# Optimization experiments

Measured on AMD Instinct MI355X. Metric: run time of the kernel, lower is better.

## Reference

```python
import jax, jax.numpy as jnp
import numpy as np

NH = 8       # num_heads
EDIM = 256   # embedding_dim (also per-head dim in this module)
BS, SQL = 4, 1024


def setup_inputs() -> dict:
    key = jax.random.key(0)
    ks = jax.random.split(key, 5)
    scale_in = 1.0 / np.sqrt(EDIM)
    scale_out = 1.0 / np.sqrt(NH * EDIM)
    return {
        "x": jax.random.normal(ks[0], (BS, SQL, EDIM), dtype=jnp.float32),
        "w_attn": jax.random.normal(ks[1], (NH * 3 * EDIM, EDIM), dtype=jnp.float32) * scale_in,
        "b_attn": jax.random.normal(ks[2], (NH * 3 * EDIM,), dtype=jnp.float32) * scale_in,
        "w_out": jax.random.normal(ks[3], (EDIM, NH * EDIM), dtype=jnp.float32) * scale_out,
        "b_out": jax.random.normal(ks[4], (EDIM,), dtype=jnp.float32) * scale_out,
    }


def reference(x, w_attn, b_attn, w_out, b_out):
    bs, sql, edim = x.shape
    nh = NH
    # projections: (bs, sql, nh*3*edim); split into Q, K, V chunks of nh*edim
    proj = x @ w_attn.T + b_attn
    q, k, v = jnp.split(proj, 3, axis=-1)
    # Faithful to torch: raw view (bs, sql, nh*edim) -> (bs, nh, sql, edim),
    # a reinterpretation of memory, NOT a transpose.
    q = q.reshape(bs, nh, sql, edim)
    k = k.reshape(bs, nh, sql, edim)
    v = v.reshape(bs, nh, sql, edim)
    # scaled dot-product scores: (bs, nh, sql, sql)
    scores = jnp.einsum("bhqd,bhkd->bhqk", q, k) / jnp.sqrt(jnp.float32(edim))
    # causal mask: -inf strictly above the diagonal (equivalent to adding triu(-inf, 1))
    causal = jnp.tril(jnp.ones((sql, sql), dtype=bool))
    scores = jnp.where(causal, scores, -jnp.inf)
    attn = jax.nn.softmax(scores, axis=-1)
    out = jnp.einsum("bhqk,bhkd->bhqd", attn, v)
    # Faithful raw view back: (bs, nh, sql, edim) -> (bs, sql, nh*edim)
    out = out.reshape(bs, sql, nh * edim)
    return out @ w_out.T + b_out
```

## Files before the change

### kernel.cpp

```cpp
#include <hip/hip_runtime.h>

#define SQL  1024
#define EDIM 256
#define NHD  8
#define NKV  (NHD * 3 * EDIM)
#define MROWS (4 * SQL)

typedef short bf16x8 __attribute__((ext_vector_type(8)));
typedef float f32x4 __attribute__((ext_vector_type(4)));

__device__ __forceinline__ unsigned short f2bf(float f) {
  unsigned u = __float_as_uint(f);
  u += 0x7fff + ((u >> 16) & 1);
  return (unsigned short)(u >> 16);
}

__device__ __forceinline__ void g2lds16(const void* g, void* l) {
  __builtin_amdgcn_global_load_lds(
      (const __attribute__((address_space(1))) unsigned int*)g,
      (__attribute__((address_space(3))) unsigned int*)l, 16, 0, 0);
}

__device__ __forceinline__ void storev(float* p, float v) { *p = v; }
__device__ __forceinline__ void storev(unsigned short* p, float v) { *p = f2bf(v); }

__global__ __launch_bounds__(256) void cast3_bf16(
    const float* __restrict__ s0, unsigned short* __restrict__ d0, int n0,
    const float* __restrict__ s1, unsigned short* __restrict__ d1, int n1,
    const float* __restrict__ s2, unsigned short* __restrict__ d2, int n2) {
  int i = blockIdx.x * 256 + threadIdx.x;
  const float* s; unsigned short* d;
  if (i < n0) { s = s0; d = d0; }
  else if (i < n0 + n1) { i -= n0; s = s1; d = d1; }
  else { i -= n0 + n1; if (i >= n2) return; s = s2; d = d2; }
  float4 a = ((const float4*)s)[2 * i];
  float4 b = ((const float4*)s)[2 * i + 1];
  union { unsigned short u[8]; ulonglong2 v; } t;
  t.u[0] = f2bf(a.x); t.u[1] = f2bf(a.y); t.u[2] = f2bf(a.z); t.u[3] = f2bf(a.w);
  t.u[4] = f2bf(b.x); t.u[5] = f2bf(b.y); t.u[6] = f2bf(b.z); t.u[7] = f2bf(b.w);
  ((ulonglong2*)d)[i] = t.v;
}

template <int BM, int BN, typename OutT>
__global__ __launch_bounds__(256) void gemm_mfma(
    const unsigned short* __restrict__ A, const unsigned short* __restrict__ B,
    const float* __restrict__ bias, OutT* __restrict__ C,
    int M, int N, int K) {
  constexpr int TM = BM / 32, TN = BN / 32;
  __shared__ __align__(16) unsigned short As[2][BM * 32];
  __shared__ __align__(16) unsigned short Bs[2][BN * 32];
  const int tid = threadIdx.x;
  const int wave = tid >> 6, lane = tid & 63;
  const int quad = lane >> 4, l16 = lane & 15;
  const int wm = (wave >> 1) * (BM / 2), wn = (wave & 1) * (BN / 2);
  const int m0 = blockIdx.x * BM, n0 = blockIdx.y * BN;
  const int sw = (l16 >> 1) & 3;

  f32x4 acc[TM][TN];
  #pragma unroll
  for (int i = 0; i < TM; i++)
    #pragma unroll
    for (int j = 0; j < TN; j++) acc[i][j] = {0.f, 0.f, 0.f, 0.f};

  auto stage = [&](int k0, int bb) {
    #pragma unroll
    for (int it = 0; it < BM / 64; it++) {
      int flat = it * 256 + tid;
      int row = flat >> 2;
      int cg = (flat & 3) ^ ((row >> 1) & 3);
      g2lds16(A + (size_t)(m0 + row) * K + k0 + cg * 8, &As[bb][flat * 8]);
    }
    #pragma unroll
    for (int it = 0; it < BN / 64; it++) {
      int flat = it * 256 + tid;
      int row = flat >> 2;
      int cg = (flat & 3) ^ ((row >> 1) & 3);
      g2lds16(B + (size_t)(n0 + row) * K + k0 + cg * 8, &Bs[bb][flat * 8]);
    }
  };

  stage(0, 0);
  __syncthreads();
  for (int k0 = 0; k0 < K; k0 += 32) {
    const int bb = (k0 >> 5) & 1;
    if (k0 + 32 < K) stage(k0 + 32, bb ^ 1);
    bf16x8 af[TM], bf[TN];
    #pragma unroll
    for (int i = 0; i < TM; i++)
      af[i] = *(const bf16x8*)&As[bb][(wm + i * 16 + l16) * 32 + (quad ^ sw) * 8];
    #pragma unroll
    for (int j = 0; j < TN; j++)
      bf[j] = *(const bf16x8*)&Bs[bb][(wn + j * 16 + l16) * 32 + (quad ^ sw) * 8];
    #pragma unroll
    for (int i = 0; i < TM; i++)
      #pragma unroll
      for (int j = 0; j < TN; j++)
        acc[i][j] = __builtin_amdgcn_mfma_f32_16x16x32_bf16(af[i], bf[j], acc[i][j], 0, 0, 0);
    __syncthreads();
  }

  #pragma unroll
  for (int i = 0; i < TM; i++) {
    #pragma unroll
    for (int r = 0; r < 4; r++) {
      int m = m0 + wm + i * 16 + quad * 4 + r;
      #pragma unroll
      for (int j = 0; j < TN; j++) {
        int n = n0 + wn + j * 16 + l16;
        storev(&C[(size_t)m * N + n], acc[i][j][r] + bias[n]);
      }
    }
  }
}

__global__ __launch_bounds__(256) void transpose_v(
    const unsigned short* __restrict__ proj, unsigned short* __restrict__ vt) {
  __shared__ unsigned short T[64][66];
  const int tid = threadIdx.x;
  const int s0 = blockIdx.x * 64, d0 = blockIdx.y * 64, bh = blockIdx.z;
  const int b = bh >> 3, h = bh & 7;
  #pragma unroll
  for (int it = 0; it < 2; it++) {
    int c = it * 256 + tid;
    int sr = c >> 3, k8 = (c & 7) * 8;
    int s = s0 + sr;
    const unsigned short* src = proj + (size_t)(b * SQL + h * 128 + (s >> 3)) * NKV
                                + 2 * 2048 + (s & 7) * 256 + d0 + k8;
    *(ulonglong2*)&T[sr][k8] = *(const ulonglong2*)src;
  }
  __syncthreads();
  #pragma unroll
  for (int it = 0; it < 2; it++) {
    int c = it * 256 + tid;
    int dr = c >> 3, s8 = (c & 7) * 8;
    unsigned short tmp[8];
    #pragma unroll
    for (int j = 0; j < 8; j++) tmp[j] = T[s8 + j][dr];
    unsigned short* dst = vt + ((size_t)bh * EDIM + d0 + dr) * SQL + s0 + s8;
    *(ulonglong2*)dst = *(ulonglong2*)tmp;
  }
}

__global__ __launch_bounds__(512, 4) void attn_mfma(
    const unsigned short* __restrict__ proj,
    const unsigned short* __restrict__ vt,
    unsigned short* __restrict__ oflat) {
  __shared__ __align__(16) unsigned short lds[37888];
  unsigned short* Ps = lds + 32768;

  const int tid = threadIdx.x;
  const int wave = tid >> 6, lane = tid & 63;
  const int quad = lane >> 4, l16 = lane & 15;
  const int qs = wave >> 1;
  const int dh = wave & 1;
  const int slot = blockIdx.x & 255, round = blockIdx.x >> 8;
  const int bh = slot & 31;
  const int jj = slot >> 5;
  const int qt = round ? jj : 15 - jj;
  const int b = bh >> 3, h = bh & 7;
  const int q0 = qt * 64;

  #pragma unroll
  for (int it = 0; it < 4; it++) {
    int c = it * 512 + tid;
    int r = c >> 5, ch = (c & 31) ^ (r & 7);
    int s = q0 + r;
    g2lds16(proj + (size_t)(b * SQL + h * 128 + (s >> 3)) * NKV + (s & 7) * 256 + ch * 8,
            lds + c * 8);
  }
  __syncthreads();
  bf16x8 aq[8];
  const int qrow = qs * 16 + l16;
  #pragma unroll
  for (int kk = 0; kk < 8; kk++)
    aq[kk] = *(const bf16x8*)&lds[qrow * 256 + ((kk * 4 + quad) ^ (qrow & 7)) * 8];
  __syncthreads();

  f32x4 o[8];
  #pragma unroll
  for (int t = 0; t < 8; t++) o[t] = {0.f, 0.f, 0.f, 0.f};
  float l_r[4] = {0.f, 0.f, 0.f, 0.f};

  auto stage = [&](int kt, int bb) {
    unsigned short* KsB = lds + bb * 16384;
    unsigned short* VtB = KsB + 8192;
    #pragma unroll
    for (int it = 0; it < 2; it++) {
      int c = it * 512 + tid;
      int r = c >> 5, ch = (c & 31) ^ (r & 7);
      int s = kt * 32 + r;
      g2lds16(proj + (size_t)(b * SQL + h * 128 + (s >> 3)) * NKV + 2048 + (s & 7) * 256 + ch * 8,
              KsB + c * 8);
    }
    #pragma unroll
    for (int it = 0; it < 2; it++) {
      int c = it * 512 + tid;
      int d = c >> 2, ch = (c & 3) ^ (d & 3);
      g2lds16(vt + ((size_t)bh * EDIM + d) * SQL + kt * 32 + ch * 8, VtB + c * 8);
    }
  };

  const int nkt = 2 * qt + 2;
  stage(0, 0);
  __syncthreads();

  for (int kt = 0; kt < nkt; kt++) {
    const int bb = kt & 1;
    if (kt + 1 < nkt) stage(kt + 1, bb ^ 1);
    const unsigned short* KsB = lds + bb * 16384;
    const unsigned short* VtB = KsB + 8192;
    const bool live = (kt * 32 <= q0 + qs * 16 + 15);

    if (live) {
      f32x4 s0 = {0.f, 0.f, 0.f, 0.f}, s1 = {0.f, 0.f, 0.f, 0.f};
      #pragma unroll
      for (int kk = 0; kk < 8; kk++) {
        int ch = (kk * 4 + quad) ^ (l16 & 7);
        bf16x8 b0 = *(const bf16x8*)&KsB[l16 * 256 + ch * 8];
        bf16x8 b1 = *(const bf16x8*)&KsB[(16 + l16) * 256 + ch * 8];
        s0 = __builtin_amdgcn_mfma_f32_16x16x32_bf16(aq[kk], b0, s0, 0, 0, 0);
        s1 = __builtin_amdgcn_mfma_f32_16x16x32_bf16(aq[kk], b1, s1, 0, 0, 0);
      }

      const int kg0 = kt * 32 + l16, kg1 = kg0 + 16;
      unsigned short* PsW = Ps + wave * 640;
      #pragma unroll
      for (int r = 0; r < 4; r++) {
        int qg = q0 + qs * 16 + quad * 4 + r;
        float p0 = (kg0 <= qg) ? exp2f(s0[r] * 0.09016844f) : 0.f;
        float p1 = (kg1 <= qg) ? exp2f(s1[r] * 0.09016844f) : 0.f;
        l_r[r] += p0 + p1;
        PsW[(quad * 4 + r) * 40 + l16]      = f2bf(p0);
        PsW[(quad * 4 + r) * 40 + 16 + l16] = f2bf(p1);
      }

      bf16x8 ap = *(const bf16x8*)&PsW[l16 * 40 + quad * 8];
      #pragma unroll
      for (int tl = 0; tl < 8; tl++) {
        const int vrow = dh * 128 + tl * 16 + l16;
        bf16x8 bv = *(const bf16x8*)&VtB[vrow * 32 + (quad ^ (l16 & 3)) * 8];
        o[tl] = __builtin_amdgcn_mfma_f32_16x16x32_bf16(ap, bv, o[tl], 0, 0, 0);
      }
    }
    __syncthreads();
  }

  #pragma unroll
  for (int r = 0; r < 4; r++) {
    float l = l_r[r];
    #pragma unroll
    for (int off = 1; off < 16; off <<= 1) l += __shfl_xor(l, off);
    float inv = 1.0f / l;
    int s = q0 + qs * 16 + quad * 4 + r;
    unsigned short* dst = oflat + (size_t)(b * SQL + h * 128 + (s >> 3)) * 2048
                          + (s & 7) * 256 + dh * 128;
    #pragma unroll
    for (int tl = 0; tl < 8; tl++)
      dst[tl * 16 + l16] = f2bf(o[tl][r] * inv);
  }
}

extern "C" void kernel_launch(void* const* d_in, const int* in_sizes, int n_in,
                              void* d_out, int out_size, void* d_ws, size_t ws_size,
                              hipStream_t stream) {
  const float* x      = (const float*)d_in[0];
  const float* w_attn = (const float*)d_in[1];
  const float* b_attn = (const float*)d_in[2];
  const float* w_out  = (const float*)d_in[3];
  const float* b_out  = (const float*)d_in[4];
  float* out = (float*)d_out;

  char* p = (char*)d_ws;
  unsigned short* proj = (unsigned short*)p;  p += (size_t)MROWS * NKV * 2;
  unsigned short* obf  = (unsigned short*)p;  p += (size_t)MROWS * 2048 * 2;
  unsigned short* vtb  = (unsigned short*)p;  p += (size_t)32 * EDIM * SQL * 2;
  unsigned short* xb   = (unsigned short*)p;  p += (size_t)MROWS * EDIM * 2;
  unsigned short* wb   = (unsigned short*)p;  p += (size_t)NKV * EDIM * 2;
  unsigned short* wob  = (unsigned short*)p;

  const int n0 = MROWS * EDIM / 8;
  const int n1 = NKV * EDIM / 8;
  const int n2 = EDIM * 2048 / 8;
  cast3_bf16<<<(n0 + n1 + n2) / 256, 256, 0, stream>>>(x, xb, n0, w_attn, wb, n1,
                                                       w_out, wob, n2);

  gemm_mfma<128, 128, unsigned short><<<dim3(MROWS / 128, NKV / 128), 256, 0, stream>>>(
      xb, wb, b_attn, proj, MROWS, NKV, EDIM);
  transpose_v<<<dim3(SQL / 64, EDIM / 64, 32), 256, 0, stream>>>(proj, vtb);
  attn_mfma<<<512, 512, 0, stream>>>(proj, vtb, obf);
  gemm_mfma<64, 64, float><<<dim3(MROWS / 64, EDIM / 64), 256, 0, stream>>>(
      obf, wob, b_out, out, MROWS, EDIM, NHD * EDIM);
}
```

Before: 172.0 us.

## Split attention waves over key tiles instead of head-dim halves, merge partial outputs

The attention kernel now gives each wave pair a different 32-key tile from a 64-key staged pair, and each wave covers the full 256-wide head dim, instead of splitting the head dim across the pair. Before, both waves recomputed the same QK scores and softmax; now each wave computes scores only for its own keys. Partial outputs and row sums are merged through LDS at the end. V is pre-transposed into a tiled, swizzled layout so a whole key pair stages with contiguous loads. The cost is doubled accumulator registers and larger LDS, lowering occupancy from 4 to 2 blocks per CU, plus an extra reduction pass.

```diff
diff --git a/kernel.cpp b/kernel.cpp
--- a/kernel.cpp
+++ b/kernel.cpp
@@ -136,23 +136,28 @@
     unsigned short tmp[8];
     #pragma unroll
     for (int j = 0; j < 8; j++) tmp[j] = T[s8 + j][dr];
-    unsigned short* dst = vt + ((size_t)bh * EDIM + d0 + dr) * SQL + s0 + s8;
+    const int d = d0 + dr;
+    const int t = (s0 + s8) >> 5;
+    const int j = (s8 >> 3) & 3;
+    const int cj = j ^ ((d >> 1) & 3);
+    unsigned short* dst = vt + (((size_t)bh * 32 + t) * 1024 + d * 4 + cj) * 8;
     *(ulonglong2*)dst = *(ulonglong2*)tmp;
   }
 }
 
-__global__ __launch_bounds__(512, 4) void attn_mfma(
+__global__ __launch_bounds__(512, 2) void attn_mfma(
     const unsigned short* __restrict__ proj,
     const unsigned short* __restrict__ vt,
     unsigned short* __restrict__ oflat) {
-  __shared__ __align__(16) unsigned short lds[37888];
-  unsigned short* Ps = lds + 32768;
+  __shared__ __align__(16) unsigned short lds[70656];
+  __shared__ float lsumX[4][16];
+  unsigned short* Ps = lds + 65536;
 
   const int tid = threadIdx.x;
   const int wave = tid >> 6, lane = tid & 63;
   const int quad = lane >> 4, l16 = lane & 15;
   const int qs = wave >> 1;
-  const int dh = wave & 1;
+  const int p  = wave & 1;
   const int slot = blockIdx.x & 255, round = blockIdx.x >> 8;
   const int bh = slot & 31;
   const int jj = slot >> 5;
@@ -160,56 +165,55 @@
   const int b = bh >> 3, h = bh & 7;
   const int q0 = qt * 64;
 
+  auto stagepair = [&](int pr, int bb) {
+    unsigned short* B = lds + bb * 32768;
+    #pragma unroll
+    for (int it = 0; it < 4; it++) {
+      int c = it * 512 + tid;
+      int r = c >> 5, ch = (c & 31) ^ (r & 7);
+      int s = pr * 64 + r;
+      g2lds16(proj + (size_t)(b * SQL + h * 128 + (s >> 3)) * NKV + 2048 + (s & 7) * 256 + ch * 8,
+              B + c * 8);
+    }
+    const unsigned short* vsrc = vt + ((size_t)bh * 32 + pr * 2) * 8192;
+    #pragma unroll
+    for (int it = 0; it < 4; it++) {
+      int c = it * 512 + tid;
+      g2lds16(vsrc + c * 8, B + 16384 + c * 8);
+    }
+  };
+
+  stagepair(0, 0);
   #pragma unroll
   for (int it = 0; it < 4; it++) {
     int c = it * 512 + tid;
     int r = c >> 5, ch = (c & 31) ^ (r & 7);
     int s = q0 + r;
     g2lds16(proj + (size_t)(b * SQL + h * 128 + (s >> 3)) * NKV + (s & 7) * 256 + ch * 8,
-            lds + c * 8);
+            lds + 32768 + c * 8);
   }
   __syncthreads();
   bf16x8 aq[8];
   const int qrow = qs * 16 + l16;
   #pragma unroll
   for (int kk = 0; kk < 8; kk++)
-    aq[kk] = *(const bf16x8*)&lds[qrow * 256 + ((kk * 4 + quad) ^ (qrow & 7)) * 8];
-  __syncthreads();
-
-  f32x4 o[8];
-  #pragma unroll
-  for (int t = 0; t < 8; t++) o[t] = {0.f, 0.f, 0.f, 0.f};
+    aq[kk] = *(const bf16x8*)&lds[32768 + qrow * 256 + ((kk * 4 + quad) ^ (qrow & 7)) * 8];
+  __syncthreads();
+
+  f32x4 o[16];
+  #pragma unroll
+  for (int t = 0; t < 16; t++) o[t] = {0.f, 0.f, 0.f, 0.f};
   float l_r[4] = {0.f, 0.f, 0.f, 0.f};
 
-  auto stage = [&](int kt, int bb) {
-    unsigned short* KsB = lds + bb * 16384;
-    unsigned short* VtB = KsB + 8192;
-    #pragma unroll
-    for (int it = 0; it < 2; it++) {
-      int c = it * 512 + tid;
-      int r = c >> 5, ch = (c & 31) ^ (r & 7);
-      int s = kt * 32 + r;
-      g2lds16(proj + (size_t)(b * SQL + h * 128 + (s >> 3)) * NKV + 2048 + (s & 7) * 256 + ch * 8,
-              KsB + c * 8);
-    }
-    #pragma unroll
-    for (int it = 0; it < 2; it++) {
-      int c = it * 512 + tid;
-      int d = c >> 2, ch = (c & 3) ^ (d & 3);
-      g2lds16(vt + ((size_t)bh * EDIM + d) * SQL + kt * 32 + ch * 8, VtB + c * 8);
-    }
-  };
-
-  const int nkt = 2 * qt + 2;
-  stage(0, 0);
-  __syncthreads();
-
-  for (int kt = 0; kt < nkt; kt++) {
-    const int bb = kt & 1;
-    if (kt + 1 < nkt) stage(kt + 1, bb ^ 1);
-    const unsigned short* KsB = lds + bb * 16384;
-    const unsigned short* VtB = KsB + 8192;
-    const bool live = (kt * 32 <= q0 + qs * 16 + 15);
+  const int np = qt + 1;
+  for (int pr = 0; pr < np; pr++) {
+    const int bb = pr & 1;
+    if (pr + 1 < np) stagepair(pr + 1, bb ^ 1);
+    unsigned short* B = lds + bb * 32768;
+    const unsigned short* KsB = B + p * 8192;
+    const unsigned short* VtB = B + 16384 + p * 8192;
+    const int my_kt = 2 * pr + p;
+    const bool live = (my_kt * 32 <= q0 + qs * 16 + 15);
 
     if (live) {
       f32x4 s0 = {0.f, 0.f, 0.f, 0.f}, s1 = {0.f, 0.f, 0.f, 0.f};
@@ -222,7 +226,7 @@
         s1 = __builtin_amdgcn_mfma_f32_16x16x32_bf16(aq[kk], b1, s1, 0, 0, 0);
       }
 
-      const int kg0 = kt * 32 + l16, kg1 = kg0 + 16;
+      const int kg0 = my_kt * 32 + l16, kg1 = kg0 + 16;
       unsigned short* PsW = Ps + wave * 640;
       #pragma unroll
       for (int r = 0; r < 4; r++) {
@@ -236,27 +240,48 @@
 
       bf16x8 ap = *(const bf16x8*)&PsW[l16 * 40 + quad * 8];
       #pragma unroll
-      for (int tl = 0; tl < 8; tl++) {
-        const int vrow = dh * 128 + tl * 16 + l16;
-        bf16x8 bv = *(const bf16x8*)&VtB[vrow * 32 + (quad ^ (l16 & 3)) * 8];
+      for (int tl = 0; tl < 16; tl++) {
+        const int d = tl * 16 + l16;
+        bf16x8 bv = *(const bf16x8*)&VtB[d * 32 + (quad ^ ((d >> 1) & 3)) * 8];
         o[tl] = __builtin_amdgcn_mfma_f32_16x16x32_bf16(ap, bv, o[tl], 0, 0, 0);
       }
     }
     __syncthreads();
   }
 
+  float lr[4];
   #pragma unroll
   for (int r = 0; r < 4; r++) {
     float l = l_r[r];
     #pragma unroll
     for (int off = 1; off < 16; off <<= 1) l += __shfl_xor(l, off);
-    float inv = 1.0f / l;
-    int s = q0 + qs * 16 + quad * 4 + r;
-    unsigned short* dst = oflat + (size_t)(b * SQL + h * 128 + (s >> 3)) * 2048
-                          + (s & 7) * 256 + dh * 128;
-    #pragma unroll
-    for (int tl = 0; tl < 8; tl++)
-      dst[tl * 16 + l16] = f2bf(o[tl][r] * inv);
+    lr[r] = l;
+  }
+  if (p == 1) {
+    f32x4* ob = (f32x4*)lds;
+    #pragma unroll
+    for (int t = 0; t < 16; t++) ob[(qs * 16 + t) * 64 + lane] = o[t];
+    if (l16 == 0) {
+      #pragma unroll
+      for (int r = 0; r < 4; r++) lsumX[qs][quad * 4 + r] = lr[r];
+    }
+  }
+  __syncthreads();
+  if (p == 0) {
+    const f32x4* ob = (const f32x4*)lds;
+    #pragma unroll
+    for (int t = 0; t < 16; t++) o[t] += ob[(qs * 16 + t) * 64 + lane];
+    float inv[4];
+    #pragma unroll
+    for (int r = 0; r < 4; r++) inv[r] = 1.0f / (lr[r] + lsumX[qs][quad * 4 + r]);
+    #pragma unroll
+    for (int r = 0; r < 4; r++) {
+      int s = q0 + qs * 16 + quad * 4 + r;
+      unsigned short* dst = oflat + (size_t)(b * SQL + h * 128 + (s >> 3)) * 2048 + (s & 7) * 256;
+      #pragma unroll
+      for (int t = 0; t < 16; t++)
+        dst[t * 16 + l16] = f2bf(o[t][r] * inv[r]);
+    }
   }
 }
 
```

Result: no change. 173.9 us (+1.1%).
